# Kernel tuning notes

Measured on AMD Instinct MI355X. Metric: run time of the kernel, lower is better.

## Reference

```python
import jax, jax.numpy as jnp
import numpy as np

# SPU activation from the RAI-2021 project: x^2 - 0.5 for x>=0, sigmoid(-x)-1 for x<0.

def spu(x):
    s = jax.nn.sigmoid(-x)
    return jnp.where(x >= 0, x * x - 0.5, s - 1.0)

def dspu(x):
    s = jax.nn.sigmoid(-x)
    return jnp.where(x >= 0, 2.0 * x, -s * (1.0 - s))

def get_homog(w, b):
    # [[w, b], [0, 1]]: maps coeff rows over layer outputs (out+1) -> coeffs over inputs (in+1)
    top = jnp.concatenate([w, b[:, None]], axis=1)
    bot = jnp.concatenate([jnp.zeros((1, w.shape[1]), w.dtype), jnp.ones((1, 1), w.dtype)], axis=1)
    return jnp.concatenate([top, bot], axis=0)

def slope_clip(l, u, w_l, w_u):
    # clip slopes into the range spanned by SPU derivatives at the interval endpoints
    k1, k2 = dspu(l), dspu(u)
    klo, khi = jnp.minimum(k1, k2), jnp.maximum(k1, k2)
    return jnp.clip(w_l, klo, khi), jnp.clip(w_u, klo, khi)

def lb_slope(l, u, w_l, w_u):
    # intercepts so that w*x+b lower/upper bounds SPU at the probe points {l, u, mid, 0}
    pts = jnp.stack([l, u, 0.5 * (l + u), jnp.clip(0.0, l, u)], axis=0)  # [4, n]
    b_l = jnp.min(spu(pts) - w_l[None, :] * pts, axis=0)
    b_u = jnp.max(spu(pts) - w_u[None, :] * pts, axis=0)
    return b_l, b_u

def back_sub(Wl, Wu, affine):
    # vectorized back-substitution: the per-row torch.where matmul collapses to
    # relu(l)@W_l + min(l,0)@W_u (and symmetrically for u)
    l, u = Wl[-1], Wu[-1]
    for i in range(len(Wl) - 2, -1, -1):
        if affine[i]:
            l = l @ Wl[i]
            u = u @ Wl[i]
        else:
            l = jnp.maximum(l, 0.0) @ Wl[i] + jnp.minimum(l, 0.0) @ Wu[i]
            u = jnp.maximum(u, 0.0) @ Wu[i] + jnp.minimum(u, 0.0) @ Wl[i]
    return l, u

def _forward(W1, b1, W2, b2, W3, b3, W4, b4, l_in, u_in,
             p_l1, p_u1, p_l2, p_u2, p_l3, p_u3, true_label):
    dt = W1.dtype
    Ws = [get_homog(W1, b1), get_homog(W2, b2), get_homog(W3, b3), get_homog(W4, b4)]
    one = jnp.ones((1, 1), dt)
    l0 = jnp.concatenate([l_in, one], axis=0)  # [d_in+1, 1]
    u0 = jnp.concatenate([u_in, one], axis=0)
    K = Ws[-1].shape[0]  # n_out + 1
    eye = jnp.eye(K, dtype=dt)
    w_out = jnp.concatenate([eye[:true_label], eye[true_label + 1:-1]], axis=0)  # [n_out-1, n_out+1]
    w_out = w_out.at[:, true_label].add(-1.0)
    spu_params = [(p_l1, p_u1), (p_l2, p_u2), (p_l3, p_u3)]
    Wl, Wu, affine = [l0], [u0], [False]
    for i in range(len(Ws)):
        Wl.append(Ws[i]); Wu.append(Ws[i]); affine.append(True)
        if i < len(Ws) - 1:
            l, u = back_sub(Wl, Wu, affine)
            lf, uf = l[:-1, 0], u[:-1, 0]
            pl, pu = spu_params[i]
            cl, cu = slope_clip(lf, uf, pl, pu)
            # torch copies clipped values into the leaf params under no_grad -> straight-through
            wl = pl + jax.lax.stop_gradient(cl - pl)
            wu = pu + jax.lax.stop_gradient(cu - pu)
            b_l, b_u = lb_slope(lf, uf, wl, wu)
            Wl.append(get_homog(jnp.diag(wl), b_l))
            Wu.append(get_homog(jnp.diag(wu), b_u))
            affine.append(False)
    Wl.append(w_out); Wu.append(w_out); affine.append(True)
    _, u = back_sub(Wl, Wu, affine)
    return u.flatten()

def setup_inputs() -> dict:
    key = jax.random.key(0)
    ks = jax.random.split(key, 10)
    d_in, h, n_out = 784, 2048, 10
    s = 0.03
    W1 = jax.random.normal(ks[0], (h, d_in), jnp.float32) * s
    b1 = jax.random.normal(ks[1], (h,), jnp.float32) * s
    W2 = jax.random.normal(ks[2], (h, h), jnp.float32) * s
    b2 = jax.random.normal(ks[3], (h,), jnp.float32) * s
    W3 = jax.random.normal(ks[4], (h, h), jnp.float32) * s
    b3 = jax.random.normal(ks[5], (h,), jnp.float32) * s
    W4 = jax.random.normal(ks[6], (n_out, h), jnp.float32) * s
    b4 = jax.random.normal(ks[7], (n_out,), jnp.float32) * s
    x = jax.random.normal(ks[8], (d_in, 1), jnp.float32)
    eps = 0.05
    return {
        'W1': W1, 'b1': b1, 'W2': W2, 'b2': b2, 'W3': W3, 'b3': b3, 'W4': W4, 'b4': b4,
        'l_in': x - eps, 'u_in': x + eps,
        'p_l1': jnp.zeros((h,), jnp.float32), 'p_u1': jnp.zeros((h,), jnp.float32),
        'p_l2': jnp.zeros((h,), jnp.float32), 'p_u2': jnp.zeros((h,), jnp.float32),
        'p_l3': jnp.zeros((h,), jnp.float32), 'p_u3': jnp.zeros((h,), jnp.float32),
        'true_label': 3,
    }

def reference(W1, b1, W2, b2, W3, b3, W4, b4, l_in, u_in,
              p_l1, p_u1, p_l2, p_u2, p_l3, p_u3, true_label):
    return _forward(W1, b1, W2, b2, W3, b3, W4, b4, l_in, u_in,
                    p_l1, p_u1, p_l2, p_u2, p_l3, p_u3, int(true_label))
```

## Files before the change

kernel.cpp:

```cpp
#include <hip/hip_runtime.h>
#include <math.h>

#define H 2048
#define DIN 784
#define DPAD 896

typedef unsigned short ushort_t;
typedef __attribute__((ext_vector_type(8))) short bf16x8;
typedef __attribute__((ext_vector_type(4))) float f32x4;
typedef __attribute__((ext_vector_type(4))) unsigned short u16x4;
union F4 { float4 v; float a[4]; };
union U4 { u16x4 v; ushort_t a[4]; };

__device__ __forceinline__ float spu_f(float x){
    if (x >= 0.0f) return x*x - 0.5f;
    float s = 1.0f / (1.0f + __expf(x));
    return s - 1.0f;
}
__device__ __forceinline__ float dspu_f(float x){
    if (x >= 0.0f) return 2.0f*x;
    float s = 1.0f / (1.0f + __expf(x));
    return -s * (1.0f - s);
}
__device__ __forceinline__ ushort_t f2bf(float x){
    unsigned u = __float_as_uint(x);
    unsigned r = (u + 0x7FFFu + ((u >> 16) & 1u)) >> 16;
    return (ushort_t)r;
}
__device__ __forceinline__ float bf2f(ushort_t h){
    return __uint_as_float((unsigned)h << 16);
}
__device__ __forceinline__ void load_lds16(const void* g, void* l){
    __builtin_amdgcn_global_load_lds((const __attribute__((address_space(1))) void*)g,
                                     (__attribute__((address_space(3))) void*)l,
                                     16, 0, 0);
}
__device__ __forceinline__ float block_reduce_256(float v, float* red){
    #pragma unroll
    for (int off = 32; off > 0; off >>= 1) v += __shfl_down(v, off, 64);
    int lane = threadIdx.x & 63, w = threadIdx.x >> 6;
    if (lane == 0) red[w] = v;
    __syncthreads();
    float t = 0.f;
    if (threadIdx.x == 0) t = red[0] + red[1] + red[2] + red[3];
    return t;
}
__device__ __forceinline__ void block_reduce2_256(float vl, float vu, float* red,
                                                  float& out_l, float& out_u){
    #pragma unroll
    for (int off = 32; off > 0; off >>= 1){
        vl += __shfl_down(vl, off, 64);
        vu += __shfl_down(vu, off, 64);
    }
    int lane = threadIdx.x & 63, w = threadIdx.x >> 6;
    if (lane == 0){ red[w] = vl; red[4 + w] = vu; }
    __syncthreads();
    if (threadIdx.x == 0){
        out_l = red[0] + red[1] + red[2] + red[3];
        out_u = red[4] + red[5] + red[6] + red[7];
    }
}
__device__ __forceinline__ void spu_relax(float l, float u, float pl, float pu,
                                          float& wl_o, float& wu_o, float& bl_o, float& bu_o){
    float k1 = dspu_f(l), k2 = dspu_f(u);
    float klo = fminf(k1, k2), khi = fmaxf(k1, k2);
    float cwl = fminf(fmaxf(pl, klo), khi);
    float cwu = fminf(fmaxf(pu, klo), khi);
    float pts[4];
    pts[0] = l; pts[1] = u; pts[2] = 0.5f*(l+u); pts[3] = fminf(fmaxf(0.f, l), u);
    float bmin = INFINITY, bmax = -INFINITY;
    #pragma unroll
    for (int t = 0; t < 4; t++){
        float sp = spu_f(pts[t]);
        bmin = fminf(bmin, sp - cwl * pts[t]);
        bmax = fmaxf(bmax, sp - cwu * pts[t]);
    }
    wl_o = cwl; wu_o = cwu; bl_o = bmin; bu_o = bmax;
}

__global__ __launch_bounds__(256) void conv_bounds1(
    const float* __restrict__ W2, ushort_t* __restrict__ T2,
    const float* __restrict__ W1, ushort_t* __restrict__ T1,
    const float* __restrict__ b1,
    const float* __restrict__ l_in, const float* __restrict__ u_in,
    const float* __restrict__ pl, const float* __restrict__ pu,
    float* __restrict__ wl, float* __restrict__ wu,
    float* __restrict__ bl, float* __restrict__ bu)
{
    int z = blockIdx.z;
    if (z < 2){
        __shared__ float tile[32][33];
        const float* W = z ? W1 : W2;
        ushort_t* T = z ? T1 : T2;
        int K = H, N = z ? DIN : H, Npad = z ? DPAD : H;
        if (blockIdx.x * 32 >= (unsigned)Npad) return;
        int n0 = blockIdx.x * 32, k0 = blockIdx.y * 32;
        int tx = threadIdx.x & 31;
        int ty = threadIdx.x >> 5;
        #pragma unroll
        for (int i = 0; i < 32; i += 8){
            int k = k0 + ty + i, n = n0 + tx;
            tile[ty + i][tx] = (k < K && n < N) ? W[(size_t)k * N + n] : 0.f;
        }
        __syncthreads();
        #pragma unroll
        for (int i = 0; i < 32; i += 8){
            int n = n0 + ty + i, k = k0 + tx;
            if (n < Npad && k < K) T[(size_t)n * K + k] = f2bf(tile[tx][ty + i]);
        }
        return;
    }
    int row = blockIdx.y * 64 + blockIdx.x;
    if (row >= H) return;
    __shared__ float red[8];
    const F4* Mr = (const F4*)(W1 + (size_t)row * DIN);
    const F4* li4 = (const F4*)l_in;
    const F4* ui4 = (const F4*)u_in;
    float accl = 0.f, accu = 0.f;
    for (int q = threadIdx.x; q < DIN/4; q += 256){
        F4 v = Mr[q], lo = li4[q], up = ui4[q];
        #pragma unroll
        for (int c = 0; c < 4; c++){
            float p = fmaxf(v.a[c], 0.f), n = fminf(v.a[c], 0.f);
            accl += p * lo.a[c] + n * up.a[c];
            accu += p * up.a[c] + n * lo.a[c];
        }
    }
    float tl, tu;
    block_reduce2_256(accl, accu, red, tl, tu);
    if (threadIdx.x == 0){
        float bb = b1[row];
        spu_relax(tl + bb, tu + bb, pl[row], pu[row],
                  wl[row], wu[row], bl[row], bu[row]);
    }
}

__global__ __launch_bounds__(256) void bounds_parts(
    const ushort_t* __restrict__ P_l, const ushort_t* __restrict__ P_u,
    const float* __restrict__ c_l, const float* __restrict__ c_u,
    const float* __restrict__ l_in, const float* __restrict__ u_in,
    const float* __restrict__ pl, const float* __restrict__ pu,
    float* __restrict__ wl, float* __restrict__ wu,
    float* __restrict__ bl, float* __restrict__ bu,
    int ncols, int ld, size_t pstride, int nparts)
{
    __shared__ float red[8];
    int row = blockIdx.x;
    const ushort_t* Ml = P_l + (size_t)row * ld;
    const ushort_t* Mu = P_u + (size_t)row * ld;
    const F4* li4 = (const F4*)l_in;
    const F4* ui4 = (const F4*)u_in;
    float accl = 0.f, accu = 0.f;
    for (int q = threadIdx.x; q < ncols/4; q += 256){
        float vl[4] = {0.f,0.f,0.f,0.f}, vu[4] = {0.f,0.f,0.f,0.f};
        for (int s = 0; s < nparts; s++){
            U4 a, b;
            a.v = *(const u16x4*)&Ml[(size_t)s * pstride + q*4];
            b.v = *(const u16x4*)&Mu[(size_t)s * pstride + q*4];
            #pragma unroll
            for (int c = 0; c < 4; c++){ vl[c] += bf2f(a.a[c]); vu[c] += bf2f(b.a[c]); }
        }
        F4 lo = li4[q], up = ui4[q];
        #pragma unroll
        for (int c = 0; c < 4; c++){
            accl += fmaxf(vl[c], 0.f) * lo.a[c] + fminf(vl[c], 0.f) * up.a[c];
            accu += fmaxf(vu[c], 0.f) * up.a[c] + fminf(vu[c], 0.f) * lo.a[c];
        }
    }
    float tl, tu;
    block_reduce2_256(accl, accu, red, tl, tu);
    if (threadIdx.x == 0){
        spu_relax(tl + c_l[row], tu + c_u[row], pl[row], pu[row],
                  wl[row], wu[row], bl[row], bu[row]);
    }
}

__global__ __launch_bounds__(256) void dapply_dual(
    const float* __restrict__ S, const float* __restrict__ c_in,
    const float* __restrict__ wl, const float* __restrict__ wu,
    const float* __restrict__ bl, const float* __restrict__ bu,
    const float* __restrict__ bias_next,
    ushort_t* __restrict__ Ml, ushort_t* __restrict__ Mu,
    float* __restrict__ cl_out, float* __restrict__ cu_out, int ncols)
{
    __shared__ float red[8];
    int row = blockIdx.x;
    const F4* S4 = (const F4*)(S + (size_t)row * ncols);
    u16x4* Ml4 = (u16x4*)(Ml + (size_t)row * ncols);
    u16x4* Mu4 = (u16x4*)(Mu + (size_t)row * ncols);
    const F4* wl4 = (const F4*)wl; const F4* wu4 = (const F4*)wu;
    const F4* bl4 = (const F4*)bl; const F4* bu4 = (const F4*)bu;
    const F4* bn4 = (const F4*)bias_next;
    float accl = 0.f, accu = 0.f;
    for (int q = threadIdx.x; q < ncols/4; q += 256){
        F4 v = S4[q], a = wl4[q], b = wu4[q], c = bl4[q], d = bu4[q], e = bn4[q];
        U4 rl, ru;
        #pragma unroll
        for (int k = 0; k < 4; k++){
            float p = fmaxf(v.a[k], 0.f), n = fminf(v.a[k], 0.f);
            float ml = p * a.a[k] + n * b.a[k];
            float mu = p * b.a[k] + n * a.a[k];
            rl.a[k] = f2bf(ml);
            ru.a[k] = f2bf(mu);
            accl += p * c.a[k] + n * d.a[k] + ml * e.a[k];
            accu += p * d.a[k] + n * c.a[k] + mu * e.a[k];
        }
        Ml4[q] = rl.v;
        Mu4[q] = ru.v;
    }
    float tl, tu;
    block_reduce2_256(accl, accu, red, tl, tu);
    if (threadIdx.x == 0){
        float cc = c_in[row];
        cl_out[row] = cc + tl;
        cu_out[row] = cc + tu;
    }
}

__global__ __launch_bounds__(256) void dapply_parts(
    const ushort_t* __restrict__ P_l, const ushort_t* __restrict__ P_u,
    const float* __restrict__ cl_in, const float* __restrict__ cu_in,
    const float* __restrict__ wl, const float* __restrict__ wu,
    const float* __restrict__ bl, const float* __restrict__ bu,
    const float* __restrict__ bias_next,
    ushort_t* __restrict__ Ml, ushort_t* __restrict__ Mu,
    float* __restrict__ cl_out, float* __restrict__ cu_out,
    int ncols, size_t pstride, int nparts)
{
    __shared__ float red[4];
    int row = blockIdx.x;
    int lu = blockIdx.y;
    const ushort_t* Sr = (lu ? P_u : P_l) + (size_t)row * ncols;
    const F4* wp4 = (const F4*)(lu ? wu : wl);
    const F4* wn4 = (const F4*)(lu ? wl : wu);
    const F4* bp4 = (const F4*)(lu ? bu : bl);
    const F4* bn4_ = (const F4*)(lu ? bl : bu);
    const F4* bb4 = (const F4*)bias_next;
    u16x4* Mr4 = (u16x4*)((lu ? Mu : Ml) + (size_t)row * ncols);
    float acc = 0.f;
    for (int q = threadIdx.x; q < ncols/4; q += 256){
        float vv[4] = {0.f,0.f,0.f,0.f};
        for (int s = 0; s < nparts; s++){
            U4 t; t.v = *(const u16x4*)&Sr[(size_t)s * pstride + q*4];
            #pragma unroll
            for (int c = 0; c < 4; c++) vv[c] += bf2f(t.a[c]);
        }
        F4 a = wp4[q], b = wn4[q], c4 = bp4[q], d = bn4_[q], e = bb4[q];
        U4 r;
        #pragma unroll
        for (int c = 0; c < 4; c++){
            float p = fmaxf(vv[c], 0.f), n = fminf(vv[c], 0.f);
            float m = p * a.a[c] + n * b.a[c];
            r.a[c] = f2bf(m);
            acc += p * c4.a[c] + n * d.a[c] + m * e.a[c];
        }
        Mr4[q] = r.v;
    }
    float t = block_reduce_256(acc, red);
    if (threadIdx.x == 0){
        if (lu) cu_out[row] = cu_in[row] + t;
        else    cl_out[row] = cl_in[row] + t;
    }
}

__global__ __launch_bounds__(256) void input_reduce(
    const float* __restrict__ M, const float* __restrict__ c,
    const float* __restrict__ pos_b, const float* __restrict__ neg_b,
    float* __restrict__ out, int ncols, int ld)
{
    __shared__ float red[4];
    int row = blockIdx.x;
    const float* Mr = M + (size_t)row * ld;
    float acc = 0.f;
    for (int j = threadIdx.x; j < ncols; j += 256){
        float v = Mr[j];
        acc += fmaxf(v, 0.f) * pos_b[j] + fminf(v, 0.f) * neg_b[j];
    }
    float t = block_reduce_256(acc, red);
    if (threadIdx.x == 0) out[row] = t + c[row];
}

#define TM 128
#define TN 128
#define TK 64
__global__ __launch_bounds__(256) void gemm_mfma_pair(
    const ushort_t* __restrict__ A_l, const ushort_t* __restrict__ A_u,
    const ushort_t* __restrict__ BT,
    ushort_t* __restrict__ C_l, ushort_t* __restrict__ C_u,
    int M, int N, int K, int ksplit, size_t part_stride)
{
    __shared__ ushort_t As[TM * TK];
    __shared__ ushort_t Bs[TN * TK];
    int z = blockIdx.z;
    int lu = z / ksplit, ks = z - lu * ksplit;
    const ushort_t* A = lu ? A_u : A_l;
    ushort_t* C = (lu ? C_u : C_l) + (size_t)ks * part_stride;
    int Kpart = K / ksplit;
    int kbeg = ks * Kpart;

    int tid  = threadIdx.x;
    int wave = tid >> 6, lane = tid & 63;
    int wm = (wave >> 1) * 64, wn = (wave & 1) * 64;
    int l16 = lane & 15, quad = lane >> 4;
    int row0 = blockIdx.y * TM, col0 = blockIdx.x * TN;

    int r_lo = tid >> 3;
    int kp = (((tid & 7) ^ (r_lo & 7)) * 8);
    const ushort_t *aSrc[4], *bSrc[4];
    ushort_t *aDst[4], *bDst[4];
    #pragma unroll
    for (int g = 0; g < 4; g++){
        aSrc[g] = A  + (size_t)(row0 + g*32 + r_lo) * K + kbeg + kp;
        bSrc[g] = BT + (size_t)(col0 + g*32 + r_lo) * K + kbeg + kp;
        aDst[g] = As + g*2048 + wave*512;
        bDst[g] = Bs + g*2048 + wave*512;
    }

    f32x4 acc[4][4];
    #pragma unroll
    for (int i = 0; i < 4; i++)
        #pragma unroll
        for (int j = 0; j < 4; j++)
            acc[i][j] = (f32x4){0.f, 0.f, 0.f, 0.f};

    for (int kk0 = 0; kk0 < Kpart; kk0 += TK){
        #pragma unroll
        for (int g = 0; g < 4; g++) load_lds16(aSrc[g], aDst[g]);
        #pragma unroll
        for (int g = 0; g < 4; g++) load_lds16(bSrc[g], bDst[g]);
        #pragma unroll
        for (int g = 0; g < 4; g++){ aSrc[g] += TK; bSrc[g] += TK; }
        __syncthreads();

        #pragma unroll
        for (int half = 0; half < 2; half++){
            bf16x8 af[4], bfv[4];
            #pragma unroll
            for (int t = 0; t < 4; t++){
                int ra = wm + t*16 + l16;
                int rb = wn + t*16 + l16;
                int ca = (half*4 + quad) ^ (ra & 7);
                int cb = (half*4 + quad) ^ (rb & 7);
                af[t]  = *(const bf16x8*)&As[ra * TK + ca * 8];
                bfv[t] = *(const bf16x8*)&Bs[rb * TK + cb * 8];
            }
            #pragma unroll
            for (int i = 0; i < 4; i++)
                #pragma unroll
                for (int j = 0; j < 4; j++)
                    acc[i][j] = __builtin_amdgcn_mfma_f32_16x16x32_bf16(af[i], bfv[j], acc[i][j], 0, 0, 0);
        }
        __syncthreads();
    }

    #pragma unroll
    for (int i = 0; i < 4; i++){
        #pragma unroll
        for (int j = 0; j < 4; j++){
            int r0 = row0 + wm + i*16 + quad*4;
            int cc = col0 + wn + j*16 + l16;
            #pragma unroll
            for (int rr = 0; rr < 4; rr++)
                C[(size_t)(r0 + rr) * N + cc] = f2bf(acc[i][j][rr]);
        }
    }
}

#define GK9 64
__global__ __launch_bounds__(64) void gemv9_fused(
    const float* __restrict__ S,
    const float* __restrict__ W4, const float* __restrict__ b4,
    const int* __restrict__ tlp, int mode_w4,
    const float* __restrict__ c_in,
    const float* __restrict__ w_pos, const float* __restrict__ w_neg,
    const float* __restrict__ b_pos, const float* __restrict__ b_neg,
    const float* __restrict__ bias_next,
    const float* __restrict__ B, int K, int N,
    float* __restrict__ C, float* __restrict__ c_out)
{
    __shared__ float Alds[9][GK9];
    int j = threadIdx.x;
    int k0 = blockIdx.y * GK9;
    int k = k0 + j;
    float wp = w_pos[k], wn = w_neg[k], bp = b_pos[k], bn = b_neg[k], bb = bias_next[k];
    int tl = mode_w4 ? *tlp : 0;
    float pc[9];
    #pragma unroll
    for (int r = 0; r < 9; r++){
        float v;
        if (mode_w4){
            int kr = r + (r >= tl ? 1 : 0);
            v = W4[(size_t)kr * K + k] - W4[(size_t)tl * K + k];
        } else {
            v = S[(size_t)r * K + k];
        }
        float p = fmaxf(v, 0.f), n = fminf(v, 0.f);
        float m = p * wp + n * wn;
        Alds[r][j] = m;
        pc[r] = p * bp + n * bn + m * bb;
    }
    if (blockIdx.x == 0){
        #pragma unroll
        for (int r = 0; r < 9; r++){
            float v = pc[r];
            #pragma unroll
            for (int o = 32; o > 0; o >>= 1) v += __shfl_down(v, o, 64);
            if (j == 0){
                if (blockIdx.y == 0)
                    v += mode_w4 ? (b4[r + (r >= tl ? 1 : 0)] - b4[tl]) : c_in[r];
                atomicAdd(&c_out[r], v);
            }
        }
    }
    __syncthreads();
    int col = blockIdx.x * GK9 + j;
    if (col < N){
        float acc[9] = {0.f,0.f,0.f,0.f,0.f,0.f,0.f,0.f,0.f};
        for (int kk = 0; kk < GK9; kk++){
            float b = B[(size_t)(k0 + kk) * N + col];
            #pragma unroll
            for (int r = 0; r < 9; r++) acc[r] += Alds[r][kk] * b;
        }
        #pragma unroll
        for (int r = 0; r < 9; r++) atomicAdd(&C[(size_t)r * N + col], acc[r]);
    }
}

extern "C" void kernel_launch(void* const* d_in, const int* in_sizes, int n_in,
                              void* d_out, int out_size, void* d_ws, size_t ws_size,
                              hipStream_t stream)
{
    const float* W1  = (const float*)d_in[0];
    const float* b1  = (const float*)d_in[1];
    const float* W2  = (const float*)d_in[2];
    const float* b2  = (const float*)d_in[3];
    const float* W3  = (const float*)d_in[4];
    const float* b3  = (const float*)d_in[5];
    const float* W4  = (const float*)d_in[6];
    const float* b4  = (const float*)d_in[7];
    const float* l_in = (const float*)d_in[8];
    const float* u_in = (const float*)d_in[9];
    const float* p_l1 = (const float*)d_in[10];
    const float* p_u1 = (const float*)d_in[11];
    const float* p_l2 = (const float*)d_in[12];
    const float* p_u2 = (const float*)d_in[13];
    const float* p_l3 = (const float*)d_in[14];
    const float* p_u3 = (const float*)d_in[15];
    const int*   tl   = (const int*)d_in[16];
    float* out = (float*)d_out;

    size_t off = 0;
    auto allocB = [&](size_t bytes) -> void* {
        void* p = (char*)d_ws + off;
        off += (bytes + 255) & ~(size_t)255;
        return p;
    };
    ushort_t* W1bt  = (ushort_t*)allocB((size_t)DPAD * H * 2);
    ushort_t* W2bt  = (ushort_t*)allocB((size_t)H * H * 2);
    ushort_t* Abf_l = (ushort_t*)allocB((size_t)H * H * 2);
    ushort_t* Abf_u = (ushort_t*)allocB((size_t)H * H * 2);
    ushort_t* P_l = (ushort_t*)allocB((size_t)2 * H * H * 2);
    ushort_t* P_u = (ushort_t*)allocB((size_t)2 * H * H * 2);
    float *wl1=(float*)allocB(H*4), *wu1=(float*)allocB(H*4), *bl1=(float*)allocB(H*4), *bu1=(float*)allocB(H*4);
    float *wl2=(float*)allocB(H*4), *wu2=(float*)allocB(H*4), *bl2=(float*)allocB(H*4), *bu2=(float*)allocB(H*4);
    float *wl3=(float*)allocB(H*4), *wu3=(float*)allocB(H*4), *bl3=(float*)allocB(H*4), *bu3=(float*)allocB(H*4);
    float *cl_a=(float*)allocB(H*4), *cl_b=(float*)allocB(H*4);
    float *cu_a=(float*)allocB(H*4), *cu_b=(float*)allocB(H*4);
    size_t zero_begin = off;
    float* F1  = (float*)allocB(9 * H * 4);
    float* F2  = (float*)allocB(9 * H * 4);
    float* F3  = (float*)allocB(9 * DIN * 4);
    float *c9b=(float*)allocB(64), *c9c=(float*)allocB(64), *c9d=(float*)allocB(64);
    size_t zero_bytes = off - zero_begin;

    const size_t ND_PART = (size_t)H * DPAD;
    const size_t NN_PART = (size_t)H * H;

    dim3 blk(256);

    hipMemsetAsync((char*)d_ws + zero_begin, 0, zero_bytes, stream);

    conv_bounds1<<<dim3(H/32, H/32, 3), blk, 0, stream>>>(
        W2, W2bt, W1, W1bt, b1, l_in, u_in, p_l1, p_u1, wl1, wu1, bl1, bu1);

    dapply_dual<<<H, blk, 0, stream>>>(W2, b2, wl1, wu1, bl1, bu1, b1,
                                       Abf_l, Abf_u, cl_a, cu_a, H);
    gemm_mfma_pair<<<dim3(DPAD/TN, H/TM, 8), blk, 0, stream>>>(
        Abf_l, Abf_u, W1bt, P_l, P_u, H, DPAD, H, 4, ND_PART);
    bounds_parts<<<H, blk, 0, stream>>>(P_l, P_u, cl_a, cu_a, l_in, u_in, p_l2, p_u2,
                                        wl2, wu2, bl2, bu2, DIN, DPAD, ND_PART, 4);

    dapply_dual<<<H, blk, 0, stream>>>(W3, b3, wl2, wu2, bl2, bu2, b2,
                                       Abf_l, Abf_u, cl_a, cu_a, H);
    gemm_mfma_pair<<<dim3(H/TN, H/TM, 4), blk, 0, stream>>>(
        Abf_l, Abf_u, W2bt, P_l, P_u, H, H, H, 2, NN_PART);
    dapply_parts<<<dim3(H, 2), blk, 0, stream>>>(P_l, P_u, cl_a, cu_a,
                                                 wl1, wu1, bl1, bu1, b1,
                                                 Abf_l, Abf_u, cl_b, cu_b, H, NN_PART, 2);
    gemm_mfma_pair<<<dim3(DPAD/TN, H/TM, 8), blk, 0, stream>>>(
        Abf_l, Abf_u, W1bt, P_l, P_u, H, DPAD, H, 4, ND_PART);
    bounds_parts<<<H, blk, 0, stream>>>(P_l, P_u, cl_b, cu_b, l_in, u_in, p_l3, p_u3,
                                        wl3, wu3, bl3, bu3, DIN, DPAD, ND_PART, 4);

    gemv9_fused<<<dim3(H/GK9, H/GK9), dim3(GK9), 0, stream>>>(
        nullptr, W4, b4, tl, 1, nullptr,
        wu3, wl3, bu3, bl3, b3, W3, H, H, F1, c9b);
    gemv9_fused<<<dim3(H/GK9, H/GK9), dim3(GK9), 0, stream>>>(
        F1, nullptr, nullptr, nullptr, 0, c9b,
        wu2, wl2, bu2, bl2, b2, W2, H, H, F2, c9c);
    gemv9_fused<<<dim3((DIN + GK9 - 1)/GK9, H/GK9), dim3(GK9), 0, stream>>>(
        F2, nullptr, nullptr, nullptr, 0, c9c,
        wu1, wl1, bu1, bl1, b1, W1, H, DIN, F3, c9d);
    input_reduce<<<9, blk, 0, stream>>>(F3, c9d, u_in, l_in, out, DIN, DIN);
}
```

Before: 351.0 us.

## Halve GEMM N-tile, reduce split-K partitions, widen dapply_parts loads

The MFMA GEMM tile goes from 128x128 to 128x64, with launch bounds raised to 4 blocks per CU. The split-K factor is halved on every GEMM launch (4 to 2, and 2 to 1), so fewer bf16 partial buffers are written and later summed by bounds_parts and dapply_parts. dapply_parts now reads 8 bf16 values per load and indexes the scale and bias vectors as scalars. This cuts partial-sum traffic and should raise occupancy, but each block now does more K work and each loaded A tile is reused across fewer output columns.

```diff
diff --git a/kernel.cpp b/kernel.cpp
--- a/kernel.cpp
+++ b/kernel.cpp
@@ -9,8 +9,10 @@
 typedef __attribute__((ext_vector_type(8))) short bf16x8;
 typedef __attribute__((ext_vector_type(4))) float f32x4;
 typedef __attribute__((ext_vector_type(4))) unsigned short u16x4;
+typedef __attribute__((ext_vector_type(8))) unsigned short u16x8;
 union F4 { float4 v; float a[4]; };
 union U4 { u16x4 v; ushort_t a[4]; };
+union U8 { u16x8 v; ushort_t a[8]; };
 
 __device__ __forceinline__ float spu_f(float x){
     if (x >= 0.0f) return x*x - 0.5f;
@@ -231,30 +233,34 @@
     int row = blockIdx.x;
     int lu = blockIdx.y;
     const ushort_t* Sr = (lu ? P_u : P_l) + (size_t)row * ncols;
-    const F4* wp4 = (const F4*)(lu ? wu : wl);
-    const F4* wn4 = (const F4*)(lu ? wl : wu);
-    const F4* bp4 = (const F4*)(lu ? bu : bl);
-    const F4* bn4_ = (const F4*)(lu ? bl : bu);
-    const F4* bb4 = (const F4*)bias_next;
-    u16x4* Mr4 = (u16x4*)((lu ? Mu : Ml) + (size_t)row * ncols);
+    const float* w_pos = lu ? wu : wl;
+    const float* w_neg = lu ? wl : wu;
+    const float* b_pos = lu ? bu : bl;
+    const float* b_neg = lu ? bl : bu;
+    u16x8* Mr8 = (u16x8*)((lu ? Mu : Ml) + (size_t)row * ncols);
     float acc = 0.f;
-    for (int q = threadIdx.x; q < ncols/4; q += 256){
-        float vv[4] = {0.f,0.f,0.f,0.f};
-        for (int s = 0; s < nparts; s++){
-            U4 t; t.v = *(const u16x4*)&Sr[(size_t)s * pstride + q*4];
-            #pragma unroll
-            for (int c = 0; c < 4; c++) vv[c] += bf2f(t.a[c]);
-        }
-        F4 a = wp4[q], b = wn4[q], c4 = bp4[q], d = bn4_[q], e = bb4[q];
-        U4 r;
-        #pragma unroll
-        for (int c = 0; c < 4; c++){
+    for (int q = threadIdx.x; q < ncols/8; q += 256){
+        float vv[8];
+        {
+            U8 t; t.v = *(const u16x8*)&Sr[q*8];
+            #pragma unroll
+            for (int c = 0; c < 8; c++) vv[c] = bf2f(t.a[c]);
+        }
+        for (int s = 1; s < nparts; s++){
+            U8 t; t.v = *(const u16x8*)&Sr[(size_t)s * pstride + q*8];
+            #pragma unroll
+            for (int c = 0; c < 8; c++) vv[c] += bf2f(t.a[c]);
+        }
+        U8 r;
+        #pragma unroll
+        for (int c = 0; c < 8; c++){
+            int j = q*8 + c;
             float p = fmaxf(vv[c], 0.f), n = fminf(vv[c], 0.f);
-            float m = p * a.a[c] + n * b.a[c];
+            float m = p * w_pos[j] + n * w_neg[j];
             r.a[c] = f2bf(m);
-            acc += p * c4.a[c] + n * d.a[c] + m * e.a[c];
-        }
-        Mr4[q] = r.v;
+            acc += p * b_pos[j] + n * b_neg[j] + m * bias_next[j];
+        }
+        Mr8[q] = r.v;
     }
     float t = block_reduce_256(acc, red);
     if (threadIdx.x == 0){
@@ -281,9 +287,9 @@
 }
 
 #define TM 128
-#define TN 128
+#define TN 64
 #define TK 64
-__global__ __launch_bounds__(256) void gemm_mfma_pair(
+__global__ __launch_bounds__(256, 4) void gemm_mfma_pair(
     const ushort_t* __restrict__ A_l, const ushort_t* __restrict__ A_u,
     const ushort_t* __restrict__ BT,
     ushort_t* __restrict__ C_l, ushort_t* __restrict__ C_u,
@@ -300,55 +306,63 @@
 
     int tid  = threadIdx.x;
     int wave = tid >> 6, lane = tid & 63;
-    int wm = (wave >> 1) * 64, wn = (wave & 1) * 64;
+    int wm = (wave >> 1) * 64, wn = (wave & 1) * 32;
     int l16 = lane & 15, quad = lane >> 4;
     int row0 = blockIdx.y * TM, col0 = blockIdx.x * TN;
 
     int r_lo = tid >> 3;
     int kp = (((tid & 7) ^ (r_lo & 7)) * 8);
-    const ushort_t *aSrc[4], *bSrc[4];
-    ushort_t *aDst[4], *bDst[4];
+    const ushort_t *aSrc[4], *bSrc[2];
+    ushort_t *aDst[4], *bDst[2];
     #pragma unroll
     for (int g = 0; g < 4; g++){
-        aSrc[g] = A  + (size_t)(row0 + g*32 + r_lo) * K + kbeg + kp;
+        aSrc[g] = A + (size_t)(row0 + g*32 + r_lo) * K + kbeg + kp;
+        aDst[g] = As + g*2048 + wave*512;
+    }
+    #pragma unroll
+    for (int g = 0; g < 2; g++){
         bSrc[g] = BT + (size_t)(col0 + g*32 + r_lo) * K + kbeg + kp;
-        aDst[g] = As + g*2048 + wave*512;
         bDst[g] = Bs + g*2048 + wave*512;
     }
 
-    f32x4 acc[4][4];
+    f32x4 acc[4][2];
     #pragma unroll
     for (int i = 0; i < 4; i++)
         #pragma unroll
-        for (int j = 0; j < 4; j++)
+        for (int j = 0; j < 2; j++)
             acc[i][j] = (f32x4){0.f, 0.f, 0.f, 0.f};
 
     for (int kk0 = 0; kk0 < Kpart; kk0 += TK){
         #pragma unroll
         for (int g = 0; g < 4; g++) load_lds16(aSrc[g], aDst[g]);
         #pragma unroll
-        for (int g = 0; g < 4; g++) load_lds16(bSrc[g], bDst[g]);
-        #pragma unroll
-        for (int g = 0; g < 4; g++){ aSrc[g] += TK; bSrc[g] += TK; }
+        for (int g = 0; g < 2; g++) load_lds16(bSrc[g], bDst[g]);
+        #pragma unroll
+        for (int g = 0; g < 4; g++) aSrc[g] += TK;
+        #pragma unroll
+        for (int g = 0; g < 2; g++) bSrc[g] += TK;
         __syncthreads();
 
         #pragma unroll
         for (int half = 0; half < 2; half++){
-            bf16x8 af[4], bfv[4];
+            bf16x8 af[4], bf[2];
             #pragma unroll
             for (int t = 0; t < 4; t++){
                 int ra = wm + t*16 + l16;
+                int sa = (half*4 + quad) ^ (ra & 7);
+                af[t] = *(const bf16x8*)&As[ra * TK + sa * 8];
+            }
+            #pragma unroll
+            for (int t = 0; t < 2; t++){
                 int rb = wn + t*16 + l16;
-                int ca = (half*4 + quad) ^ (ra & 7);
-                int cb = (half*4 + quad) ^ (rb & 7);
-                af[t]  = *(const bf16x8*)&As[ra * TK + ca * 8];
-                bfv[t] = *(const bf16x8*)&Bs[rb * TK + cb * 8];
+                int sb = (half*4 + quad) ^ (rb & 7);
+                bf[t] = *(const bf16x8*)&Bs[rb * TK + sb * 8];
             }
             #pragma unroll
             for (int i = 0; i < 4; i++)
                 #pragma unroll
-                for (int j = 0; j < 4; j++)
-                    acc[i][j] = __builtin_amdgcn_mfma_f32_16x16x32_bf16(af[i], bfv[j], acc[i][j], 0, 0, 0);
+                for (int j = 0; j < 2; j++)
+                    acc[i][j] = __builtin_amdgcn_mfma_f32_16x16x32_bf16(af[i], bf[j], acc[i][j], 0, 0, 0);
         }
         __syncthreads();
     }
@@ -356,7 +370,7 @@
     #pragma unroll
     for (int i = 0; i < 4; i++){
         #pragma unroll
-        for (int j = 0; j < 4; j++){
+        for (int j = 0; j < 2; j++){
             int r0 = row0 + wm + i*16 + quad*4;
             int cc = col0 + wn + j*16 + l16;
             #pragma unroll
@@ -485,22 +499,22 @@
 
     dapply_dual<<<H, blk, 0, stream>>>(W2, b2, wl1, wu1, bl1, bu1, b1,
                                        Abf_l, Abf_u, cl_a, cu_a, H);
-    gemm_mfma_pair<<<dim3(DPAD/TN, H/TM, 8), blk, 0, stream>>>(
-        Abf_l, Abf_u, W1bt, P_l, P_u, H, DPAD, H, 4, ND_PART);
+    gemm_mfma_pair<<<dim3(DPAD/TN, H/TM, 4), blk, 0, stream>>>(
+        Abf_l, Abf_u, W1bt, P_l, P_u, H, DPAD, H, 2, ND_PART);
     bounds_parts<<<H, blk, 0, stream>>>(P_l, P_u, cl_a, cu_a, l_in, u_in, p_l2, p_u2,
-                                        wl2, wu2, bl2, bu2, DIN, DPAD, ND_PART, 4);
+                                        wl2, wu2, bl2, bu2, DIN, DPAD, ND_PART, 2);
 
     dapply_dual<<<H, blk, 0, stream>>>(W3, b3, wl2, wu2, bl2, bu2, b2,
                                        Abf_l, Abf_u, cl_a, cu_a, H);
-    gemm_mfma_pair<<<dim3(H/TN, H/TM, 4), blk, 0, stream>>>(
-        Abf_l, Abf_u, W2bt, P_l, P_u, H, H, H, 2, NN_PART);
+    gemm_mfma_pair<<<dim3(H/TN, H/TM, 2), blk, 0, stream>>>(
+        Abf_l, Abf_u, W2bt, P_l, P_u, H, H, H, 1, NN_PART);
     dapply_parts<<<dim3(H, 2), blk, 0, stream>>>(P_l, P_u, cl_a, cu_a,
                                                  wl1, wu1, bl1, bu1, b1,
-                                                 Abf_l, Abf_u, cl_b, cu_b, H, NN_PART, 2);
-    gemm_mfma_pair<<<dim3(DPAD/TN, H/TM, 8), blk, 0, stream>>>(
-        Abf_l, Abf_u, W1bt, P_l, P_u, H, DPAD, H, 4, ND_PART);
+                                                 Abf_l, Abf_u, cl_b, cu_b, H, NN_PART, 1);
+    gemm_mfma_pair<<<dim3(DPAD/TN, H/TM, 4), blk, 0, stream>>>(
+        Abf_l, Abf_u, W1bt, P_l, P_u, H, DPAD, H, 2, ND_PART);
     bounds_parts<<<H, blk, 0, stream>>>(P_l, P_u, cl_b, cu_b, l_in, u_in, p_l3, p_u3,
-                                        wl3, wu3, bl3, bu3, DIN, DPAD, ND_PART, 4);
+                                        wl3, wu3, bl3, bu3, DIN, DPAD, ND_PART, 2);
 
     gemv9_fused<<<dim3(H/GK9, H/GK9), dim3(GK9), 0, stream>>>(
         nullptr, W4, b4, tl, 1, nullptr,
```

Measured after the change: 329.0 us. 6.3% less time.
